# Performance work log

Measured on AMD Instinct MI355X. Metric: run time of the kernel, lower is better.

Reference implementation:

```python
import jax, jax.numpy as jnp
import numpy as np

B, S, D, H = 2, 2048, 1024, 16
HD = D // H  # head dim = 64


def setup_inputs() -> dict:
    key = jax.random.key(0)
    ks = jax.random.split(key, 8)
    s = 0.02
    return {
        "Q": jax.random.normal(ks[0], (B, S, D), jnp.float32),
        "K": jax.random.normal(ks[1], (B, S, D), jnp.float32),
        "V": jax.random.normal(ks[2], (B, S, D), jnp.float32),
        "mask": jax.random.randint(ks[3], (1, 1, S, S), 0, 2, jnp.int32),
        "Wq": jax.random.normal(ks[4], (D, D), jnp.float32) * s,
        "bq": jnp.zeros((D,), jnp.float32),
        "Wk": jax.random.normal(ks[5], (D, D), jnp.float32) * s,
        "bk": jnp.zeros((D,), jnp.float32),
        "Wv": jax.random.normal(ks[6], (D, D), jnp.float32) * s,
        "bv": jnp.zeros((D,), jnp.float32),
        "Wo": jax.random.normal(ks[7], (D, D), jnp.float32) * s,
        "bo": jnp.zeros((D,), jnp.float32),
    }


def reference(Q, K, V, mask, Wq, bq, Wk, bk, Wv, bv, Wo, bo):
    b = Q.shape[0]
    # QKV projections, split into heads: [B,S,D] -> [B,H,S,HD]
    q = (Q @ Wq + bq).reshape(b, -1, H, HD).transpose(0, 2, 1, 3)
    k = (K @ Wk + bk).reshape(b, -1, H, HD).transpose(0, 2, 1, 3)
    v = (V @ Wv + bv).reshape(b, -1, H, HD).transpose(0, 2, 1, 3)
    # scaled dot-product attention with full [B,H,S,S] scores (as in source)
    scale = jnp.sqrt(jnp.asarray(HD, q.dtype))
    scores = jnp.einsum("bhqd,bhkd->bhqk", q, k) / scale
    scores = jnp.where(mask == 0, -jnp.inf, scores)
    attn = jax.nn.softmax(scores, axis=-1)
    ctx = jnp.einsum("bhqk,bhkd->bhqd", attn, v)
    # merge heads and output projection
    concat = ctx.transpose(0, 2, 1, 3).reshape(b, -1, H * HD)
    return concat @ Wo + bo
```

## Files before the change

### kernel.cpp

```cpp
#include <hip/hip_runtime.h>


using s8v = __attribute__((ext_vector_type(8))) short;
using f4v = __attribute__((ext_vector_type(4))) float;
using f16v = __attribute__((ext_vector_type(16))) float;
typedef unsigned long long u64;

__device__ __forceinline__ unsigned short f2bf(float f) {
  union { float f; unsigned int u; } v; v.f = f;
  return (unsigned short)((v.u + 0x7fffu + ((v.u >> 16) & 1u)) >> 16);
}

__device__ __forceinline__ unsigned pkbf(float lo, float hi2) {
  return __builtin_amdgcn_perm(__float_as_uint(hi2), __float_as_uint(lo), 0x07060302);
}

__device__ __forceinline__ void gll16(const void* g, void* l) {
  __builtin_amdgcn_global_load_lds(
      (const __attribute__((address_space(1))) unsigned int*)g,
      (__attribute__((address_space(3))) unsigned int*)l, 16, 0, 0);
}

__global__ void prep_kernel(const float* __restrict__ Q, const float* __restrict__ K,
                            const float* __restrict__ V,
                            unsigned short* __restrict__ qb, unsigned short* __restrict__ kb,
                            unsigned short* __restrict__ vb,
                            const float* __restrict__ W0, const float* __restrict__ W1,
                            const float* __restrict__ W2, const float* __restrict__ W3,
                            unsigned short* __restrict__ T0, unsigned short* __restrict__ T1,
                            unsigned short* __restrict__ T2, unsigned short* __restrict__ T3,
                            const int* __restrict__ mask, unsigned* __restrict__ bmw) {
  __shared__ unsigned short t[64][72];
  const int bid = blockIdx.x, tid = threadIdx.x;
  if (bid < 12288) {
    int z = bid >> 12;
    int idx = (bid & 4095) * 256 + tid;
    const float* in = (z == 0) ? Q : (z == 1) ? K : V;
    unsigned short* out = (z == 0) ? qb : (z == 1) ? kb : vb;
    float4 v = ((const float4*)in)[idx];
    ushort4 o;
    o.x = f2bf(v.x); o.y = f2bf(v.y); o.z = f2bf(v.z); o.w = f2bf(v.w);
    ((ushort4*)out)[idx] = o;
  } else if (bid < 13312) {
    int b = bid - 12288;
    int z = b >> 8, rem = b & 255;
    int k0 = (rem >> 4) * 64, n0 = (rem & 15) * 64;
    const float* W = (z == 0) ? W0 : (z == 1) ? W1 : (z == 2) ? W2 : W3;
    unsigned short* Wt = (z == 0) ? T0 : (z == 1) ? T1 : (z == 2) ? T2 : T3;
    for (int p = 0; p < 4; ++p) {
      int idx = p * 256 + tid;
      int row = idx >> 4, c4 = idx & 15;
      float4 v = *(const float4*)&W[(size_t)(k0 + row) * 1024 + n0 + c4 * 4];
      t[row][c4 * 4 + 0] = f2bf(v.x);
      t[row][c4 * 4 + 1] = f2bf(v.y);
      t[row][c4 * 4 + 2] = f2bf(v.z);
      t[row][c4 * 4 + 3] = f2bf(v.w);
    }
    __syncthreads();
    for (int p = 0; p < 2; ++p) {
      int idx = p * 256 + tid;
      int j = idx >> 3, c8 = idx & 7;
      unsigned short tmp[8];
      for (int i = 0; i < 8; ++i) tmp[i] = t[c8 * 8 + i][j];
      uint4 o;
      o.x = tmp[0] | ((unsigned)tmp[1] << 16);
      o.y = tmp[2] | ((unsigned)tmp[3] << 16);
      o.z = tmp[4] | ((unsigned)tmp[5] << 16);
      o.w = tmp[6] | ((unsigned)tmp[7] << 16);
      *(uint4*)&Wt[(size_t)(n0 + j) * 1024 + k0 + c8 * 8] = o;
    }
  } else {
    int g = (bid - 13312) * 256 + tid;
    int widx = g & 15, hi = (g >> 4) & 1, l31 = (g >> 5) & 31;
    int it = (g >> 10) & 31, rowblk = g >> 15;
    int ni = widx >> 3, kcl = (widx >> 2) & 1, e = widx & 3;
    int kk = 64 * it + 32 * ni + 16 * kcl + 4 * hi + (e >> 1) * 8 + (e & 1) * 2;
    int qrow = rowblk * 32 + l31;
    const int* mrow = mask + (size_t)qrow * 2048 + kk;
    unsigned wd = (mrow[0] ? 0xFFFFu : 0u) | (mrow[1] ? 0xFFFF0000u : 0u);
    bmw[g] = wd;
  }
}

__global__ __launch_bounds__(256) void proj3_kernel(
    const unsigned short* __restrict__ A0, const unsigned short* __restrict__ A1,
    const unsigned short* __restrict__ A2,
    const unsigned short* __restrict__ W0, const unsigned short* __restrict__ W1,
    const unsigned short* __restrict__ W2,
    const float* __restrict__ b0, const float* __restrict__ b1, const float* __restrict__ b2,
    unsigned short* __restrict__ oq, unsigned short* __restrict__ ok,
    unsigned short* __restrict__ ovt) {
  const int z = blockIdx.z;
  const unsigned short* A  = (z == 0) ? A0 : (z == 1) ? A1 : A2;
  const unsigned short* Wt = (z == 0) ? W0 : (z == 1) ? W1 : W2;
  const float* bias        = (z == 0) ? b0 : (z == 1) ? b1 : b2;

  __shared__ __align__(16) union SH {
    unsigned short KB[3][8192];
    unsigned short Ls[128][136];
  } sh;

  const int tid = threadIdx.x;
  const int lane = tid & 63, w = tid >> 6, ln = lane & 15, quad = lane >> 4;
  const int wm = (w & 1) * 64, wn = (w >> 1) * 64;
  const int m0 = blockIdx.x * 128, n0 = blockIdx.y * 128;

  const int slr = lane >> 2;
  const int schunk = (lane & 3) ^ ((lane >> 3) & 3);
  const int cfrag = (quad ^ ((ln >> 1) & 3)) * 8;

  auto STAGE = [&](int buf, int kt) {
    gll16(&A[(size_t)(m0 + w * 32 + slr) * 1024 + kt + schunk * 8],       &sh.KB[buf][(w * 32) * 32]);
    gll16(&A[(size_t)(m0 + w * 32 + 16 + slr) * 1024 + kt + schunk * 8],  &sh.KB[buf][(w * 32 + 16) * 32]);
    gll16(&Wt[(size_t)(n0 + w * 32 + slr) * 1024 + kt + schunk * 8],      &sh.KB[buf][4096 + (w * 32) * 32]);
    gll16(&Wt[(size_t)(n0 + w * 32 + 16 + slr) * 1024 + kt + schunk * 8], &sh.KB[buf][4096 + (w * 32 + 16) * 32]);
  };

  f4v zero = {0.f, 0.f, 0.f, 0.f};
  f4v acc[4][4];
  for (int mi = 0; mi < 4; ++mi)
    for (int ni = 0; ni < 4; ++ni) acc[mi][ni] = zero;

  STAGE(0, 0);
  STAGE(1, 32);
  asm volatile("s_waitcnt vmcnt(4)" ::: "memory");
  __builtin_amdgcn_s_barrier();
  __builtin_amdgcn_sched_barrier(0);

  int cur = 0;
  for (int step = 0; step < 32; ++step) {
    if (step < 30) {
      const int nb = (cur == 0) ? 2 : cur - 1;
      STAGE(nb, step * 32 + 64);
    }
    const unsigned short* Asb = &sh.KB[cur][0];
    const unsigned short* Bsb = &sh.KB[cur][4096];
    s8v a[4], b[4];
    for (int mi = 0; mi < 4; ++mi) a[mi] = *(const s8v*)&Asb[(wm + mi * 16 + ln) * 32 + cfrag];
    for (int ni = 0; ni < 4; ++ni) b[ni] = *(const s8v*)&Bsb[(wn + ni * 16 + ln) * 32 + cfrag];
    if (z < 2) {
      for (int mi = 0; mi < 4; ++mi)
        for (int ni = 0; ni < 4; ++ni)
          acc[mi][ni] = __builtin_amdgcn_mfma_f32_16x16x32_bf16(a[mi], b[ni], acc[mi][ni], 0, 0, 0);
    } else {
      for (int mi = 0; mi < 4; ++mi)
        for (int ni = 0; ni < 4; ++ni)
          acc[mi][ni] = __builtin_amdgcn_mfma_f32_16x16x32_bf16(b[ni], a[mi], acc[mi][ni], 0, 0, 0);
    }
    if (step < 30)       asm volatile("s_waitcnt vmcnt(4)" ::: "memory");
    else if (step == 30) asm volatile("s_waitcnt vmcnt(0)" ::: "memory");
    if (step < 31) {
      __builtin_amdgcn_s_barrier();
      __builtin_amdgcn_sched_barrier(0);
    }
    cur = (cur == 2) ? 0 : cur + 1;
  }
  __syncthreads();

  if (z < 2) {
    const float qscale = (z == 0) ? 0.18033688f : 1.0f;
    for (int mi = 0; mi < 4; ++mi) {
      int row = wm + mi * 16 + quad * 4;
      for (int ni = 0; ni < 4; ++ni) {
        int col = wn + ni * 16 + ln;
        float bvv = bias[n0 + col];
        for (int r = 0; r < 4; ++r)
          sh.Ls[row + r][col] = f2bf((acc[mi][ni][r] + bvv) * qscale);
      }
    }
  } else {
    for (int ni = 0; ni < 4; ++ni) {
      for (int r = 0; r < 4; ++r) {
        int colw = wn + ni * 16 + quad * 4 + r;
        float bvv = bias[n0 + colw];
        for (int mi = 0; mi < 4; ++mi) {
          int rowg = wm + mi * 16 + ln;
          sh.Ls[colw][rowg] = f2bf(acc[mi][ni][r] + bvv);
        }
      }
    }
  }
  __syncthreads();

  if (z < 2) {
    unsigned short* outp = (z == 0) ? oq : ok;
    for (int p = 0; p < 8; ++p) {
      int row = p * 16 + (tid >> 4);
      int cg  = tid & 15;
      uint4 vv = *(const uint4*)&sh.Ls[row][cg * 8];
      int rb = m0 + row, b_ = rb >> 11, s = rb & 2047;
      int colg = n0 + cg * 8, h = colg >> 6, hd = colg & 63;
      *(uint4*)&outp[(((size_t)(b_ * 16 + h)) * 2048 + s) * 64 + hd] = vv;
    }
  } else {
    for (int p = 0; p < 8; ++p) {
      int rr = p * 16 + (tid >> 4);
      int cg = tid & 15;
      uint4 vv = *(const uint4*)&sh.Ls[rr][cg * 8];
      int colw = n0 + rr, h = colw >> 6, hd = colw & 63;
      int sg = m0 + cg * 8, b_ = sg >> 11, ss = sg & 2047;
      *(uint4*)&ovt[(((size_t)(b_ * 16 + h)) * 64 + hd) * 2048 + ss] = vv;
    }
  }
}

#define FLASH_ITER(i, SIN0, SIN1, SOUT0, SOUT1)                                 \
  {                                                                             \
    const int cur = (i) & 1;                                                    \
    uint4 nA, nB, nC, nD;                                                       \
    if ((i) < 31) {                                                             \
      const uint4* m4 = (const uint4*)(mwp + ((i) + 1) * 1024);                 \
      nA = m4[0]; nB = m4[1]; nC = m4[2]; nD = m4[3];                           \
    }                                                                           \
          \
    __builtin_amdgcn_s_setprio(1);                                              \
    if ((i) < 31) {                                                             \
      s8v ak0 = *(const s8v*)&k_s[cur ^ 1][l31][hi * 8];                        \
      s8v ak1 = *(const s8v*)&k_s[cur ^ 1][32 + l31][hi * 8];                   \
      SOUT0 = __builtin_amdgcn_mfma_f32_32x32x16_bf16(ak0, qf[0], zf, 0, 0, 0); \
      SOUT1 = __builtin_amdgcn_mfma_f32_32x32x16_bf16(ak1, qf[0], zf, 0, 0, 0); \
      _Pragma("unroll")                                                         \
      for (int c = 1; c < 4; ++c) {                                             \
        ak0 = *(const s8v*)&k_s[cur ^ 1][l31][c * 16 + hi * 8];                 \
        ak1 = *(const s8v*)&k_s[cur ^ 1][32 + l31][c * 16 + hi * 8];            \
        SOUT0 = __builtin_amdgcn_mfma_f32_32x32x16_bf16(ak0, qf[c], SOUT0, 0, 0, 0); \
        SOUT1 = __builtin_amdgcn_mfma_f32_32x32x16_bf16(ak1, qf[c], SOUT1, 0, 0, 0); \
      }                                                                         \
    }                                                                           \
    __builtin_amdgcn_s_setprio(0);                                              \
         \
    s8v pf[4];                                                                  \
    _Pragma("unroll")                                                           \
    for (int ni = 0; ni < 2; ++ni) {                                            \
      const f16v sv = ni ? SIN1 : SIN0;                                         \
      _Pragma("unroll")                                                         \
      for (int kcl = 0; kcl < 2; ++kcl) {                                       \
        const int rb = 8 * kcl;                                                 \
        const uint4 mw = ni ? (kcl ? mwD : mwC) : (kcl ? mwB : mwA);            \
        unsigned x0 = pkbf(__builtin_amdgcn_exp2f(sv[rb + 0]),                  \
                           __builtin_amdgcn_exp2f(sv[rb + 1])) & mw.x;          \
        unsigned x1 = pkbf(__builtin_amdgcn_exp2f(sv[rb + 2]),                  \
                           __builtin_amdgcn_exp2f(sv[rb + 3])) & mw.y;          \
        unsigned y0 = pkbf(__builtin_amdgcn_exp2f(sv[rb + 4]),                  \
                           __builtin_amdgcn_exp2f(sv[rb + 5])) & mw.z;          \
        unsigned y1 = pkbf(__builtin_amdgcn_exp2f(sv[rb + 6]),                  \
                           __builtin_amdgcn_exp2f(sv[rb + 7])) & mw.w;          \
        asm("v_permlane32_swap_b32 %0, %1" : "+v"(x0), "+v"(y0));               \
        asm("v_permlane32_swap_b32 %0, %1" : "+v"(x1), "+v"(y1));               \
        union { uint4 u; s8v v; } cv;                                           \
        cv.u = make_uint4(x0, x1, y0, y1);                                      \
        pf[ni * 2 + kcl] = cv.v;                                                \
      }                                                                         \
    }                                                                           \
                                              \
    __builtin_amdgcn_s_setprio(1);                                              \
    _Pragma("unroll")                                                           \
    for (int kc = 0; kc < 4; ++kc)                                              \
      lac = __builtin_amdgcn_mfma_f32_32x32x16_bf16(pf[kc], ones, lac, 0, 0, 0);\
    _Pragma("unroll")                                                           \
    for (int kc = 0; kc < 4; ++kc) {                                            \
      s8v bv0 = *(const s8v*)&v_s[cur][l31][kc * 16 + hi * 8];                  \
      s8v bv1 = *(const s8v*)&v_s[cur][32 + l31][kc * 16 + hi * 8];             \
      o0 = __builtin_amdgcn_mfma_f32_32x32x16_bf16(pf[kc], bv0, o0, 0, 0, 0);   \
      o1 = __builtin_amdgcn_mfma_f32_32x32x16_bf16(pf[kc], bv1, o1, 0, 0, 0);   \
    }                                                                           \
    __builtin_amdgcn_s_setprio(0);                                              \
       \
                \
    __builtin_amdgcn_sched_barrier(0);                                          \
    __builtin_amdgcn_s_barrier();                                               \
    __builtin_amdgcn_sched_barrier(0);                                          \
    if ((i) < 30) WRITET(cur);                         \
    if ((i) < 29) LOADT((i) + 3);         \
     \
    asm volatile("s_waitcnt lgkmcnt(0)" ::: "memory");                          \
    __builtin_amdgcn_sched_barrier(0);                                          \
    __builtin_amdgcn_s_barrier();                                               \
    __builtin_amdgcn_sched_barrier(0);                                          \
    mwA = nA; mwB = nB; mwC = nC; mwD = nD;                                     \
  }

__global__ __launch_bounds__(256, 2) void flash_kernel(
    const unsigned short* __restrict__ q, const unsigned short* __restrict__ k,
    const unsigned short* __restrict__ vt, const unsigned* __restrict__ bmw,
    unsigned short* __restrict__ ctx) {
  __shared__ __align__(16) unsigned short k_s[2][64][72];
  __shared__ __align__(16) unsigned short v_s[2][64][72];

  const int tid = threadIdx.x;
  const int lane = tid & 63, w = tid >> 6;
  const int l31 = lane & 31, hi = lane >> 5;
  const int q0 = blockIdx.x * 128;
  const int bh = blockIdx.y;
  const unsigned short* qg  = q  + ((size_t)bh * 2048 + q0) * 64;
  const unsigned short* kgb = k  + (size_t)bh * 2048 * 64;
  const unsigned short* vgb = vt + (size_t)bh * 64 * 2048;
  const unsigned* mwp = bmw + (size_t)(blockIdx.x * 4 + w) * 32768 + l31 * 32 + hi * 16;

  const int qrow = w * 32 + l31;
  s8v qf[4];
#pragma unroll
  for (int c = 0; c < 4; ++c)
    qf[c] = *(const s8v*)&qg[(size_t)qrow * 64 + c * 16 + hi * 8];

  s8v ones;
#pragma unroll
  for (int i = 0; i < 8; ++i) ones[i] = (short)0x3F80;
  f16v zf;
#pragma unroll
  for (int i = 0; i < 16; ++i) zf[i] = 0.f;

  const int srow = tid >> 3, sc8 = tid & 7;

  uint4 kr0, kr1, vr0, vr1;
  auto LOADT = [&](int it) {
    const int kk = it * 64;
    kr0 = *(const uint4*)&kgb[(size_t)(kk + srow) * 64 + sc8 * 8];
    kr1 = *(const uint4*)&kgb[(size_t)(kk + srow + 32) * 64 + sc8 * 8];
    vr0 = *(const uint4*)&vgb[(size_t)srow * 2048 + kk + sc8 * 8];
    vr1 = *(const uint4*)&vgb[(size_t)(srow + 32) * 2048 + kk + sc8 * 8];
  };
  auto WRITET = [&](int b) {
    *(uint4*)&k_s[b][srow][sc8 * 8] = kr0;
    *(uint4*)&k_s[b][srow + 32][sc8 * 8] = kr1;
    *(uint4*)&v_s[b][srow][sc8 * 8] = vr0;
    *(uint4*)&v_s[b][srow + 32][sc8 * 8] = vr1;
  };

  LOADT(0); WRITET(0);
  LOADT(1); WRITET(1);
  LOADT(2);
  __syncthreads();

  uint4 mwA, mwB, mwC, mwD;
  {
    const uint4* m4 = (const uint4*)mwp;
    mwA = m4[0]; mwB = m4[1]; mwC = m4[2]; mwD = m4[3];
  }

  f16v sA0, sA1, sB0, sB1;
  {
    s8v ak0 = *(const s8v*)&k_s[0][l31][hi * 8];
    s8v ak1 = *(const s8v*)&k_s[0][32 + l31][hi * 8];
    sA0 = __builtin_amdgcn_mfma_f32_32x32x16_bf16(ak0, qf[0], zf, 0, 0, 0);
    sA1 = __builtin_amdgcn_mfma_f32_32x32x16_bf16(ak1, qf[0], zf, 0, 0, 0);
#pragma unroll
    for (int c = 1; c < 4; ++c) {
      ak0 = *(const s8v*)&k_s[0][l31][c * 16 + hi * 8];
      ak1 = *(const s8v*)&k_s[0][32 + l31][c * 16 + hi * 8];
      sA0 = __builtin_amdgcn_mfma_f32_32x32x16_bf16(ak0, qf[c], sA0, 0, 0, 0);
      sA1 = __builtin_amdgcn_mfma_f32_32x32x16_bf16(ak1, qf[c], sA1, 0, 0, 0);
    }
  }

  f16v o0, o1, lac;
#pragma unroll
  for (int i = 0; i < 16; ++i) { o0[i] = 0.f; o1[i] = 0.f; lac[i] = 0.f; }

  for (int ii = 0; ii < 16; ++ii) {
    const int i0 = ii * 2;
    FLASH_ITER(i0,     sA0, sA1, sB0, sB1);
    FLASH_ITER(i0 + 1, sB0, sB1, sA0, sA1);
  }

  const int b_ = bh >> 4, h = bh & 15;
#pragma unroll
  for (int r = 0; r < 16; ++r) {
    const int ql = (r & 3) + 8 * (r >> 2) + 4 * hi;
    const float inv = 1.f / lac[r];
    const int srw = q0 + w * 32 + ql;
    const size_t base = ((size_t)b_ * 2048 + srw) * 1024 + h * 64;
    ctx[base + l31] = f2bf(o0[r] * inv);
    ctx[base + 32 + l31] = f2bf(o1[r] * inv);
  }
}

__global__ __launch_bounds__(256) void gemm_out_kernel(
    const unsigned short* __restrict__ A, const unsigned short* __restrict__ Wt,
    const float* __restrict__ bias, float* __restrict__ out) {
  __shared__ __align__(16) unsigned short As[3][2048];
  __shared__ __align__(16) unsigned short Bs[3][4096];

  const int tid = threadIdx.x;
  const int lane = tid & 63, w = tid >> 6, ln = lane & 15, quad = lane >> 4;
  const int wm = (w & 1) * 32, wn = (w >> 1) * 64;
  const int m0 = blockIdx.x * 64, n0 = blockIdx.y * 128;

  const int slr = lane >> 2;
  const int schunk = (lane & 3) ^ ((lane >> 3) & 3);
  const int cfrag = (quad ^ ((ln >> 1) & 3)) * 8;

  auto STAGE = [&](int buf, int kt) {
    gll16(&A[(size_t)(m0 + w * 16 + slr) * 1024 + kt + schunk * 8],       &As[buf][(w * 16) * 32]);
    gll16(&Wt[(size_t)(n0 + w * 32 + slr) * 1024 + kt + schunk * 8],      &Bs[buf][(w * 32) * 32]);
    gll16(&Wt[(size_t)(n0 + w * 32 + 16 + slr) * 1024 + kt + schunk * 8], &Bs[buf][(w * 32 + 16) * 32]);
  };

  f4v zero = {0.f, 0.f, 0.f, 0.f};
  f4v acc[2][4];
  for (int mi = 0; mi < 2; ++mi)
    for (int ni = 0; ni < 4; ++ni) acc[mi][ni] = zero;

  STAGE(0, 0);
  STAGE(1, 32);
  asm volatile("s_waitcnt vmcnt(3)" ::: "memory");
  __builtin_amdgcn_s_barrier();
  __builtin_amdgcn_sched_barrier(0);

  int cur = 0;
  for (int step = 0; step < 32; ++step) {
    if (step < 30) {
      const int nb = (cur == 0) ? 2 : cur - 1;
      STAGE(nb, step * 32 + 64);
    }
    s8v a[2], b[4];
    for (int mi = 0; mi < 2; ++mi) a[mi] = *(const s8v*)&As[cur][(wm + mi * 16 + ln) * 32 + cfrag];
    for (int ni = 0; ni < 4; ++ni) b[ni] = *(const s8v*)&Bs[cur][(wn + ni * 16 + ln) * 32 + cfrag];
    for (int mi = 0; mi < 2; ++mi)
      for (int ni = 0; ni < 4; ++ni)
        acc[mi][ni] = __builtin_amdgcn_mfma_f32_16x16x32_bf16(a[mi], b[ni], acc[mi][ni], 0, 0, 0);
    if (step < 30)       asm volatile("s_waitcnt vmcnt(3)" ::: "memory");
    else if (step == 30) asm volatile("s_waitcnt vmcnt(0)" ::: "memory");
    if (step < 31) {
      __builtin_amdgcn_s_barrier();
      __builtin_amdgcn_sched_barrier(0);
    }
    cur = (cur == 2) ? 0 : cur + 1;
  }

  for (int mi = 0; mi < 2; ++mi) {
    int rb = m0 + wm + mi * 16 + quad * 4;
    for (int ni = 0; ni < 4; ++ni) {
      int col = n0 + wn + ni * 16 + ln;
      float bvv = bias[col];
      for (int r = 0; r < 4; ++r)
        out[(size_t)(rb + r) * 1024 + col] = acc[mi][ni][r] + bvv;
    }
  }
}

extern "C" void kernel_launch(void* const* d_in, const int* in_sizes, int n_in,
                              void* d_out, int out_size, void* d_ws, size_t ws_size,
                              hipStream_t stream) {
  const float* Q  = (const float*)d_in[0];
  const float* K  = (const float*)d_in[1];
  const float* V  = (const float*)d_in[2];
  const int* mask = (const int*)d_in[3];
  const float* Wq = (const float*)d_in[4];
  const float* bq = (const float*)d_in[5];
  const float* Wk = (const float*)d_in[6];
  const float* bk = (const float*)d_in[7];
  const float* Wv = (const float*)d_in[8];
  const float* bv = (const float*)d_in[9];
  const float* Wo = (const float*)d_in[10];
  const float* bo = (const float*)d_in[11];
  float* out = (float*)d_out;

  char* ws = (char*)d_ws;
  const size_t MB = 1u << 20;
  unsigned short* qb  = (unsigned short*)(ws + 0 * MB);
  unsigned short* kb  = (unsigned short*)(ws + 8 * MB);
  unsigned short* vb  = (unsigned short*)(ws + 16 * MB);
  unsigned short* wqt = (unsigned short*)(ws + 24 * MB);
  unsigned short* wkt = (unsigned short*)(ws + 26 * MB);
  unsigned short* wvt = (unsigned short*)(ws + 28 * MB);
  unsigned short* wot = (unsigned short*)(ws + 30 * MB);
  unsigned short* qh  = (unsigned short*)(ws + 32 * MB);
  unsigned short* kh  = (unsigned short*)(ws + 40 * MB);
  unsigned short* vth = (unsigned short*)(ws + 48 * MB);
  unsigned* bmw       = (unsigned*)(ws + 56 * MB);
  unsigned short* ctx = (unsigned short*)(ws + 16 * MB);

  prep_kernel<<<21504, 256, 0, stream>>>(Q, K, V, qb, kb, vb,
                                         Wq, Wk, Wv, Wo, wqt, wkt, wvt, wot,
                                         mask, bmw);
  proj3_kernel<<<dim3(32, 8, 3), 256, 0, stream>>>(qb, kb, vb, wqt, wkt, wvt,
                                                   bq, bk, bv, qh, kh, vth);
  flash_kernel<<<dim3(16, 32), 256, 0, stream>>>(qh, kh, vth, bmw, ctx);
  gemm_out_kernel<<<dim3(64, 8), 256, 0, stream>>>(ctx, wot, bo, out);
}
```

Before: 246.9 us.

## Swizzle block IDs across XCDs and coarsen prep kernel work per block

Remaps linear block IDs in the projection, flash-attention and output GEMM kernels so that blocks sharing the same operand tiles land on the same XCD (stride-8 swizzle), improving L2 reuse on the multi-die GPU. The prep kernel now processes 8 elements per thread in a loop, cutting its grid from 21504 to 3584 blocks to reduce launch and scheduling overhead. The swizzles assume exact grid sizes and the 8-XCD round-robin dispatch.

```diff
diff --git a/kernel.cpp b/kernel.cpp
--- a/kernel.cpp
+++ b/kernel.cpp
@@ -32,17 +32,21 @@
                             const int* __restrict__ mask, unsigned* __restrict__ bmw) {
   __shared__ unsigned short t[64][72];
   const int bid = blockIdx.x, tid = threadIdx.x;
-  if (bid < 12288) {
-    int z = bid >> 12;
-    int idx = (bid & 4095) * 256 + tid;
+  if (bid < 1536) {
+    int z = bid >> 9;
+    int base = (bid & 511) * 2048;
     const float* in = (z == 0) ? Q : (z == 1) ? K : V;
     unsigned short* out = (z == 0) ? qb : (z == 1) ? kb : vb;
-    float4 v = ((const float4*)in)[idx];
-    ushort4 o;
-    o.x = f2bf(v.x); o.y = f2bf(v.y); o.z = f2bf(v.z); o.w = f2bf(v.w);
-    ((ushort4*)out)[idx] = o;
-  } else if (bid < 13312) {
-    int b = bid - 12288;
+#pragma unroll
+    for (int j = 0; j < 8; ++j) {
+      int idx = base + j * 256 + tid;
+      float4 v = ((const float4*)in)[idx];
+      ushort4 o;
+      o.x = f2bf(v.x); o.y = f2bf(v.y); o.z = f2bf(v.z); o.w = f2bf(v.w);
+      ((ushort4*)out)[idx] = o;
+    }
+  } else if (bid < 2560) {
+    int b = bid - 1536;
     int z = b >> 8, rem = b & 255;
     int k0 = (rem >> 4) * 64, n0 = (rem & 15) * 64;
     const float* W = (z == 0) ? W0 : (z == 1) ? W1 : (z == 2) ? W2 : W3;
@@ -70,15 +74,19 @@
       *(uint4*)&Wt[(size_t)(n0 + j) * 1024 + k0 + c8 * 8] = o;
     }
   } else {
-    int g = (bid - 13312) * 256 + tid;
-    int widx = g & 15, hi = (g >> 4) & 1, l31 = (g >> 5) & 31;
-    int it = (g >> 10) & 31, rowblk = g >> 15;
-    int ni = widx >> 3, kcl = (widx >> 2) & 1, e = widx & 3;
-    int kk = 64 * it + 32 * ni + 16 * kcl + 4 * hi + (e >> 1) * 8 + (e & 1) * 2;
-    int qrow = rowblk * 32 + l31;
-    const int* mrow = mask + (size_t)qrow * 2048 + kk;
-    unsigned wd = (mrow[0] ? 0xFFFFu : 0u) | (mrow[1] ? 0xFFFF0000u : 0u);
-    bmw[g] = wd;
+    int b = bid - 2560;
+#pragma unroll
+    for (int j = 0; j < 8; ++j) {
+      int g = b * 2048 + j * 256 + tid;
+      int widx = g & 15, hi = (g >> 4) & 1, l31 = (g >> 5) & 31;
+      int it = (g >> 10) & 31, rowblk = g >> 15;
+      int ni = widx >> 3, kcl = (widx >> 2) & 1, e = widx & 3;
+      int kk = 64 * it + 32 * ni + 16 * kcl + 4 * hi + (e >> 1) * 8 + (e & 1) * 2;
+      int qrow = rowblk * 32 + l31;
+      const int* mrow = mask + (size_t)qrow * 2048 + kk;
+      unsigned wd = (mrow[0] ? 0xFFFFu : 0u) | (mrow[1] ? 0xFFFF0000u : 0u);
+      bmw[g] = wd;
+    }
   }
 }
 
@@ -90,7 +98,11 @@
     const float* __restrict__ b0, const float* __restrict__ b1, const float* __restrict__ b2,
     unsigned short* __restrict__ oq, unsigned short* __restrict__ ok,
     unsigned short* __restrict__ ovt) {
-  const int z = blockIdx.z;
+  const int orig = blockIdx.z * 256 + blockIdx.y * 32 + blockIdx.x;
+  const int swz = (orig & 7) * 96 + (orig >> 3);
+  const int z = swz >> 8;
+  const int bx = swz & 31, by = (swz >> 5) & 7;
+
   const unsigned short* A  = (z == 0) ? A0 : (z == 1) ? A1 : A2;
   const unsigned short* Wt = (z == 0) ? W0 : (z == 1) ? W1 : W2;
   const float* bias        = (z == 0) ? b0 : (z == 1) ? b1 : b2;
@@ -103,7 +115,7 @@
   const int tid = threadIdx.x;
   const int lane = tid & 63, w = tid >> 6, ln = lane & 15, quad = lane >> 4;
   const int wm = (w & 1) * 64, wn = (w >> 1) * 64;
-  const int m0 = blockIdx.x * 128, n0 = blockIdx.y * 128;
+  const int m0 = bx * 128, n0 = by * 128;
 
   const int slr = lane >> 2;
   const int schunk = (lane & 3) ^ ((lane >> 3) & 3);
@@ -265,8 +277,8 @@
       o1 = __builtin_amdgcn_mfma_f32_32x32x16_bf16(pf[kc], bv1, o1, 0, 0, 0);   \
     }                                                                           \
     __builtin_amdgcn_s_setprio(0);                                              \
-       \
-                \
+           \
+                                \
     __builtin_amdgcn_sched_barrier(0);                                          \
     __builtin_amdgcn_s_barrier();                                               \
     __builtin_amdgcn_sched_barrier(0);                                          \
@@ -290,12 +302,14 @@
   const int tid = threadIdx.x;
   const int lane = tid & 63, w = tid >> 6;
   const int l31 = lane & 31, hi = lane >> 5;
-  const int q0 = blockIdx.x * 128;
-  const int bh = blockIdx.y;
+  const int orig = blockIdx.y * 16 + blockIdx.x;
+  const int swzid = (orig & 7) * 64 + (orig >> 3);
+  const int bx = swzid & 15, bh = swzid >> 4;
+  const int q0 = bx * 128;
   const unsigned short* qg  = q  + ((size_t)bh * 2048 + q0) * 64;
   const unsigned short* kgb = k  + (size_t)bh * 2048 * 64;
   const unsigned short* vgb = vt + (size_t)bh * 64 * 2048;
-  const unsigned* mwp = bmw + (size_t)(blockIdx.x * 4 + w) * 32768 + l31 * 32 + hi * 16;
+  const unsigned* mwp = bmw + (size_t)(bx * 4 + w) * 32768 + l31 * 32 + hi * 16;
 
   const int qrow = w * 32 + l31;
   s8v qf[4];
@@ -384,7 +398,9 @@
   const int tid = threadIdx.x;
   const int lane = tid & 63, w = tid >> 6, ln = lane & 15, quad = lane >> 4;
   const int wm = (w & 1) * 32, wn = (w >> 1) * 64;
-  const int m0 = blockIdx.x * 64, n0 = blockIdx.y * 128;
+  const int orig = blockIdx.y * 64 + blockIdx.x;
+  const int swzid = (orig & 7) * 64 + (orig >> 3);
+  const int m0 = (swzid & 63) * 64, n0 = (swzid >> 6) * 128;
 
   const int slr = lane >> 2;
   const int schunk = (lane & 3) ^ ((lane >> 3) & 3);
@@ -471,9 +487,9 @@
   unsigned* bmw       = (unsigned*)(ws + 56 * MB);
   unsigned short* ctx = (unsigned short*)(ws + 16 * MB);
 
-  prep_kernel<<<21504, 256, 0, stream>>>(Q, K, V, qb, kb, vb,
-                                         Wq, Wk, Wv, Wo, wqt, wkt, wvt, wot,
-                                         mask, bmw);
+  prep_kernel<<<3584, 256, 0, stream>>>(Q, K, V, qb, kb, vb,
+                                        Wq, Wk, Wv, Wo, wqt, wkt, wvt, wot,
+                                        mask, bmw);
   proj3_kernel<<<dim3(32, 8, 3), 256, 0, stream>>>(qb, kb, vb, wqt, wkt, wvt,
                                                    bq, bk, bv, qh, kh, vth);
   flash_kernel<<<dim3(16, 32), 256, 0, stream>>>(qh, kh, vth, bmw, ctx);
```

New measurement: 245.8 us. No clear change (-0.4%).
